# Kernel tuning notes

Measured on AMD Instinct MI355X. Metric: run time of the kernel, lower is better.

The kernel has to match this reference:

```python
import jax, jax.numpy as jnp
import numpy as np

N = 100000      # nodes
E = 1600000     # edges (avg degree 16)
F_IN = 128      # num_node_features
H = 64          # hidden_features
C = 40          # num_classes


def _glorot(key, shape):
    lim = np.sqrt(6.0 / (shape[0] + shape[1]))
    return jax.random.uniform(key, shape, jnp.float32, -lim, lim)


def setup_inputs() -> dict:
    key = jax.random.key(0)
    k = jax.random.split(key, 4)
    x = jax.random.normal(k[0], (N, F_IN), dtype=jnp.float32)
    edge_index = jax.random.randint(k[1], (2, E), 0, N, dtype=jnp.int32)
    W1 = _glorot(k[2], (F_IN, H))
    b1 = jnp.zeros((H,), jnp.float32)
    W2 = _glorot(k[3], (H, C))
    b2 = jnp.zeros((C,), jnp.float32)
    return {"x": x, "edge_index": edge_index, "W1": W1, "b1": b1, "W2": W2, "b2": b2}


def _gcn_conv(x, src, dst, dinv_sqrt, W, b):
    # GCNConv: out = D^{-1/2} (A + I) D^{-1/2} (x W) + b
    h = x @ W                                        # [N, out]
    norm = dinv_sqrt[src] * dinv_sqrt[dst]           # [E+N]
    msg = h[src] * norm[:, None]                     # gather + scale
    agg = jax.ops.segment_sum(msg, dst, num_segments=N)
    return agg + b


def reference(x, edge_index, W1, b1, W2, b2):
    loop = jnp.arange(N, dtype=edge_index.dtype)
    src = jnp.concatenate([edge_index[0], loop])     # add self-loops
    dst = jnp.concatenate([edge_index[1], loop])
    # degree of A + I (counts in-edges at destination, incl. self-loop)
    deg = jax.ops.segment_sum(jnp.ones_like(dst, jnp.float32), dst, num_segments=N)
    dinv_sqrt = jax.lax.rsqrt(deg)                   # deg >= 1 due to self-loops

    h = _gcn_conv(x, src, dst, dinv_sqrt, W1, b1)
    h = jax.nn.relu(h)
    # F.dropout(training=self.training) is identity in eval mode
    out = _gcn_conv(h, src, dst, dinv_sqrt, W2, b2)
    return out
```

## Files before the change

### kernel.cpp

```cpp
#include <hip/hip_runtime.h>
#include <hip/hip_fp16.h>
#include <cstdint>
#include <cstddef>

#define NPB_SHIFT 8
#define NPB (1 << NPB_SHIFT)
#define CHUNK 4096
#define BCAP 6144

typedef _Float16 half8_t __attribute__((ext_vector_type(8)));
typedef _Float16 half4_t __attribute__((ext_vector_type(4)));
typedef _Float16 half2_t __attribute__((ext_vector_type(2)));
typedef float floatx4 __attribute__((ext_vector_type(4)));

#define H2(u) __builtin_bit_cast(half2_t, (u))


__global__ __launch_bounds__(256) void k_partition(const int* __restrict__ src,
                                                   const int* __restrict__ dst,
                                                   int* __restrict__ bfill,
                                                   unsigned* __restrict__ tmp,
                                                   int E, int nbuck) {
  __shared__ int cnt[512];
  __shared__ int lbase[512];
  __shared__ int gdelta[512];
  __shared__ int cur[512];
  __shared__ int ps[256];
  __shared__ unsigned sval[CHUNK];
  __shared__ unsigned short sbid[CHUNK];
  int tid = threadIdx.x;
  int cbase = blockIdx.x * CHUNK;
  for (int i = tid; i < 512; i += 256) cnt[i] = 0;
  __syncthreads();
  int s[16], d[16];
  bool valid[16];
#pragma unroll
  for (int u = 0; u < 16; ++u) {
    int e = cbase + u * 256 + tid;
    valid[u] = e < E;
    s[u] = valid[u] ? src[e] : 0;
    d[u] = valid[u] ? dst[e] : 0;
    if (valid[u]) atomicAdd(&cnt[d[u] >> NPB_SHIFT], 1);
  }
  __syncthreads();
  int c0 = cnt[2 * tid], c1 = cnt[2 * tid + 1];
  int p = c0 + c1;
  ps[tid] = p;
  __syncthreads();
  for (int off = 1; off < 256; off <<= 1) {
    int t = (tid >= off) ? ps[tid - off] : 0;
    __syncthreads();
    ps[tid] += t;
    __syncthreads();
  }
  int ep = ps[tid] - p;
  lbase[2 * tid] = ep;
  lbase[2 * tid + 1] = ep + c0;
  __syncthreads();
  for (int i = tid; i < 512; i += 256) {
    cur[i] = lbase[i];
    if (cnt[i]) gdelta[i] = atomicAdd(&bfill[i], cnt[i]) - lbase[i];
  }
  __syncthreads();
#pragma unroll
  for (int u = 0; u < 16; ++u) {
    if (valid[u]) {
      int b = d[u] >> NPB_SHIFT;
      int r = atomicAdd(&cur[b], 1);
      sval[r] = ((unsigned)s[u] << NPB_SHIFT) | (unsigned)(d[u] & (NPB - 1));
      sbid[r] = (unsigned short)b;
    }
  }
  __syncthreads();
  int nv = min(CHUNK, E - cbase);
  for (int i = tid; i < nv; i += 256) {
    unsigned v = sval[i];
    int b = sbid[i];
    tmp[(size_t)b * BCAP + (gdelta[b] + i)] = v;
  }
}

__global__ __launch_bounds__(256) void k_csr_build(const unsigned* __restrict__ tmp,
                                                   const int* __restrict__ bfill,
                                                   float* __restrict__ dinv,
                                                   int* __restrict__ offset,
                                                   int* __restrict__ ssrc,
                                                   int N, int E, int nbuck) {
  __shared__ int cnt[NPB];
  __shared__ int scan[NPB];
  __shared__ int fillL[NPB];
  __shared__ int bs[512];
  __shared__ int ps[256];
  int b = blockIdx.x, tid = threadIdx.x;
  int nbase = b << NPB_SHIFT;
  int nloc = min(NPB, N - nbase);
  cnt[tid] = 0;
  bs[tid] = (tid < nbuck) ? bfill[tid] : 0;
  bs[tid + 256] = (tid + 256 < nbuck) ? bfill[tid + 256] : 0;
  __syncthreads();
  int c0 = bs[2 * tid], c1 = bs[2 * tid + 1];
  int pp = c0 + c1;
  ps[tid] = pp;
  __syncthreads();
  for (int off = 1; off < 256; off <<= 1) {
    int t = (tid >= off) ? ps[tid - off] : 0;
    __syncthreads();
    ps[tid] += t;
    __syncthreads();
  }
  int ep = ps[tid] - pp;
  bs[2 * tid] = ep;
  bs[2 * tid + 1] = ep + c0;
  __syncthreads();
  int ebeg = bs[b];
  int cntB = bfill[b];
  int sbeg = b * BCAP;
  int send = sbeg + cntB;
  for (int j = sbeg + tid; j < send; j += 256) atomicAdd(&cnt[tmp[j] & (NPB - 1)], 1);
  __syncthreads();
  int v = cnt[tid];
  scan[tid] = v;
  __syncthreads();
  for (int off = 1; off < NPB; off <<= 1) {
    int t = (tid >= off) ? scan[tid - off] : 0;
    __syncthreads();
    scan[tid] += t;
    __syncthreads();
  }
  int myoff = ebeg + scan[tid] - v;
  fillL[tid] = myoff;
  if (tid < nloc) {
    offset[nbase + tid] = myoff;
    dinv[nbase + tid] = rsqrtf((float)(v + 1));
  }
  if (b == nbuck - 1 && tid == NPB - 1) offset[N] = ebeg + scan[tid];
  __syncthreads();
  int j = sbeg + tid;
  for (; j + 3 * 256 < send; j += 4 * 256) {
    unsigned p[4];
#pragma unroll
    for (int u = 0; u < 4; ++u) p[u] = tmp[j + u * 256];
#pragma unroll
    for (int u = 0; u < 4; ++u) {
      int pos = atomicAdd(&fillL[p[u] & (NPB - 1)], 1);
      ssrc[pos] = (int)(p[u] >> NPB_SHIFT);
    }
  }
  for (; j < send; j += 256) {
    unsigned p = tmp[j];
    int pos = atomicAdd(&fillL[p & (NPB - 1)], 1);
    ssrc[pos] = (int)(p >> NPB_SHIFT);
  }
}

template <int K, int COLS, int MT, int KC, int OS, typename XT>
__global__ __launch_bounds__(256) void k_gemm_mfma(const XT* __restrict__ x,
                                                   const float* __restrict__ W,
                                                   const float* __restrict__ dinv,
                                                   _Float16* __restrict__ out, int n) {
  int lane = threadIdx.x & 63;
  int quad = lane >> 4;
  int l15 = lane & 15;
  int gwave = (blockIdx.x * blockDim.x + threadIdx.x) >> 6;
  int nwave = (gridDim.x * blockDim.x) >> 6;
  int ntiles = (n + 15) >> 4;

  half8_t afrag[MT][KC];
#pragma unroll
  for (int m = 0; m < MT; ++m) {
    int colw = m * 16 + l15;
    if (colw > COLS - 1) colw = COLS - 1;
#pragma unroll
    for (int c = 0; c < KC; ++c) {
#pragma unroll
      for (int j = 0; j < 8; ++j) {
        int kk = c * 32 + quad * 8 + j;
        afrag[m][c][j] = (_Float16)W[kk * COLS + colw];
      }
    }
  }

  for (int tile = gwave; tile < ntiles; tile += nwave) {
    int node0 = tile << 4;
    int nodeB = node0 + l15;
    int nodeC = nodeB < n ? nodeB : n - 1;
    const XT* xr = x + (size_t)nodeC * K;
    float dv = dinv[nodeC];
    half8_t bfrag[KC];
#pragma unroll
    for (int c = 0; c < KC; ++c) {
      if constexpr (sizeof(XT) == 4) {
        float4 lo = *(const float4*)(xr + c * 32 + quad * 8);
        float4 hi = *(const float4*)(xr + c * 32 + quad * 8 + 4);
        bfrag[c][0] = (_Float16)lo.x; bfrag[c][1] = (_Float16)lo.y;
        bfrag[c][2] = (_Float16)lo.z; bfrag[c][3] = (_Float16)lo.w;
        bfrag[c][4] = (_Float16)hi.x; bfrag[c][5] = (_Float16)hi.y;
        bfrag[c][6] = (_Float16)hi.z; bfrag[c][7] = (_Float16)hi.w;
      } else {
        bfrag[c] = *(const half8_t*)(xr + c * 32 + quad * 8);
      }
    }
    floatx4 acc[MT];
#pragma unroll
    for (int m = 0; m < MT; ++m) acc[m] = (floatx4){0.f, 0.f, 0.f, 0.f};
#pragma unroll
    for (int c = 0; c < KC; ++c)
#pragma unroll
      for (int m = 0; m < MT; ++m)
        acc[m] = __builtin_amdgcn_mfma_f32_16x16x32_f16(afrag[m][c], bfrag[c], acc[m], 0, 0, 0);

    if (nodeB < n) {
#pragma unroll
      for (int m = 0; m < MT; ++m) {
        int colBase = m * 16 + quad * 4;
        if (colBase < COLS) {
          half4_t hv = {(_Float16)(acc[m][0] * dv), (_Float16)(acc[m][1] * dv),
                        (_Float16)(acc[m][2] * dv), (_Float16)(acc[m][3] * dv)};
          *(half4_t*)(out + (size_t)nodeB * OS + colBase) = hv;
        }
      }
    }
  }
}


__device__ __forceinline__ void addacc(half2_t* acc, uint4 r) {
  acc[0] += H2(r.x); acc[1] += H2(r.y); acc[2] += H2(r.z); acc[3] += H2(r.w);
}

template <int F, int S8, bool RELU, bool OUT_HALF>
__global__ __launch_bounds__(256) void k_agg_v4(const uint4* __restrict__ g8,
                                                const int* __restrict__ offset,
                                                const int* __restrict__ ssrc,
                                                const float* __restrict__ dinv,
                                                const float* __restrict__ bias,
                                                void* __restrict__ outp, int n) {
  constexpr int F8 = F / 8;
  int lane = threadIdx.x & 63;
  int g = lane >> 3;
  int t = lane & 7;
  int wave = (blockIdx.x * blockDim.x + threadIdx.x) >> 6;
  int nb = wave * 4;
  if (nb >= n) return;
  bool tv = t < F8;

  uint4 sv[4];
#pragma unroll
  for (int w = 0; w < 4; ++w) {
    int node = nb + w;
    int nc = node < n ? node : n - 1;
    sv[w] = (tv && g == 0 && node < n) ? g8[(size_t)nc * S8 + t]
                                       : make_uint4(0, 0, 0, 0);
  }

  int jj[4], ee[4];
  float di[4];
#pragma unroll
  for (int w = 0; w < 4; ++w) {
    int node = nb + w;
    bool nv = node < n;
    int nc = nv ? node : n - 1;
    int b0 = offset[nc];
    int b1 = offset[nc + 1];
    jj[w] = b0;
    ee[w] = nv ? b1 : b0;
    di[w] = dinv[nc];
  }

  half2_t acc[4][4];
#pragma unroll
  for (int w = 0; w < 4; ++w) {
#pragma unroll
    for (int k = 0; k < 4; ++k) acc[w][k] = H2(0u);
    addacc(acc[w], sv[w]);
  }

  for (;;) {
    bool a0[4], a1[4];
    bool any = false;
#pragma unroll
    for (int w = 0; w < 4; ++w) {
      a0[w] = jj[w] + 8 <= ee[w];
      a1[w] = jj[w] + 16 <= ee[w];
      any = any || a0[w];
    }
    if (!any) break;
    int s0[4], s1[4];
#pragma unroll
    for (int w = 0; w < 4; ++w) {
      s0[w] = a0[w] ? ssrc[jj[w] + g] : 0;
      s1[w] = a1[w] ? ssrc[jj[w] + 8 + g] : 0;
    }
    uint4 r0[4], r1[4];
#pragma unroll
    for (int w = 0; w < 4; ++w) {
      r0[w] = (a0[w] && tv) ? g8[(size_t)s0[w] * S8 + t] : make_uint4(0, 0, 0, 0);
      r1[w] = (a1[w] && tv) ? g8[(size_t)s1[w] * S8 + t] : make_uint4(0, 0, 0, 0);
    }
#pragma unroll
    for (int w = 0; w < 4; ++w) {
      addacc(acc[w], r0[w]);
      addacc(acc[w], r1[w]);
      jj[w] += a1[w] ? 16 : (a0[w] ? 8 : 0);
    }
  }

  {
    int rem[4];
    uint4 rv[4];
#pragma unroll
    for (int w = 0; w < 4; ++w) {
      rem[w] = ee[w] - jj[w];
      int gi = (g < rem[w]) ? g : (rem[w] - 1);
      int sW = rem[w] > 0 ? ssrc[jj[w] + gi] : 0;
      rv[w] = (tv && g < rem[w]) ? g8[(size_t)sW * S8 + t] : make_uint4(0, 0, 0, 0);
    }
#pragma unroll
    for (int w = 0; w < 4; ++w) addacc(acc[w], rv[w]);
  }

#pragma unroll
  for (int w = 0; w < 4; ++w) {
#pragma unroll
    for (int k = 0; k < 4; ++k) {
      int u = __builtin_bit_cast(int, acc[w][k]);
      acc[w][k] += H2((unsigned)__shfl_xor(u, 8));
      u = __builtin_bit_cast(int, acc[w][k]);
      acc[w][k] += H2((unsigned)__shfl_xor(u, 16));
      u = __builtin_bit_cast(int, acc[w][k]);
      acc[w][k] += H2((unsigned)__shfl_xor(u, 32));
    }
    int node = nb + w;
    if (node < n && lane < F8) {
      float f[8];
#pragma unroll
      for (int k = 0; k < 4; ++k) {
        f[2 * k] = (float)acc[w][k][0];
        f[2 * k + 1] = (float)acc[w][k][1];
      }
      const float* bb = bias + lane * 8;
      float o[8];
#pragma unroll
      for (int j = 0; j < 8; ++j) {
        o[j] = fmaf(f[j], di[w], bb[j]);
        if (RELU) o[j] = fmaxf(o[j], 0.f);
      }
      if (OUT_HALF) {
        _Float16* op = (_Float16*)outp + (size_t)node * F + lane * 8;
        half2_t p0 = {(_Float16)o[0], (_Float16)o[1]};
        half2_t p1 = {(_Float16)o[2], (_Float16)o[3]};
        half2_t p2 = {(_Float16)o[4], (_Float16)o[5]};
        half2_t p3 = {(_Float16)o[6], (_Float16)o[7]};
        uint4 wv;
        wv.x = __builtin_bit_cast(unsigned, p0);
        wv.y = __builtin_bit_cast(unsigned, p1);
        wv.z = __builtin_bit_cast(unsigned, p2);
        wv.w = __builtin_bit_cast(unsigned, p3);
        *(uint4*)op = wv;
      } else {
        float* op = (float*)outp + (size_t)node * F + lane * 8;
        *(float4*)op = make_float4(o[0], o[1], o[2], o[3]);
        *(float4*)(op + 4) = make_float4(o[4], o[5], o[6], o[7]);
      }
    }
  }
}


extern "C" void kernel_launch(void* const* d_in, const int* in_sizes, int n_in,
                              void* d_out, int out_size, void* d_ws, size_t ws_size,
                              hipStream_t stream) {
  const float* x  = (const float*)d_in[0];
  const int*   ei = (const int*)d_in[1];
  const float* W1 = (const float*)d_in[2];
  const float* b1 = (const float*)d_in[3];
  const float* W2 = (const float*)d_in[4];
  const float* b2 = (const float*)d_in[5];
  float* out = (float*)d_out;

  const int F_IN = 128, HID = 64, C = 40;
  int N = in_sizes[0] / F_IN;
  int E = in_sizes[1] / 2;
  const int* src = ei;
  const int* dst = ei + E;
  int nbuck = (N + NPB - 1) >> NPB_SHIFT;

  char* w = (char*)d_ws;
  size_t o = 0;
  auto alloc = [&](size_t bytes) -> void* {
    void* p = w + o;
    o = (o + bytes + 255) & ~(size_t)255;
    return p;
  };
  float*    dinv   = (float*)alloc((size_t)N * 4);
  int*      offset = (int*)alloc((size_t)(N + 1) * 4);
  int*      bfill  = (int*)alloc(512 * 4);
  unsigned* tmp    = (unsigned*)alloc((size_t)nbuck * BCAP * 4);
  int*      ssrc   = (int*)alloc((size_t)E * 4);
  _Float16* g1     = (_Float16*)alloc((size_t)N * HID * 2);
  _Float16* h1     = (_Float16*)alloc((size_t)N * HID * 2);
  _Float16* g2     = (_Float16*)alloc((size_t)N * C * 2);

  dim3 b256(256);

  hipMemsetAsync(bfill, 0, 512 * 4, stream);
  k_partition<<<dim3((E + CHUNK - 1) / CHUNK), b256, 0, stream>>>(src, dst, bfill, tmp, E, nbuck);
  k_csr_build<<<dim3(nbuck), b256, 0, stream>>>(tmp, bfill, dinv, offset, ssrc, N, E, nbuck);

  k_gemm_mfma<128, 64, 4, 4, 64, float><<<dim3(1536), b256, 0, stream>>>(x, W1, dinv, g1, N);
  k_agg_v4<64, 8, true, true><<<dim3((N + 15) / 16), b256, 0, stream>>>(
      (const uint4*)g1, offset, ssrc, dinv, b1, h1, N);

  k_gemm_mfma<64, 40, 3, 2, 40, _Float16><<<dim3(1536), b256, 0, stream>>>(h1, W2, dinv, g2, N);
  k_agg_v4<40, 5, false, false><<<dim3((N + 15) / 16), b256, 0, stream>>>(
      (const uint4*)g2, offset, ssrc, dinv, b2, out, N);
}
```

Measured before the change: 250.4 us.

## Fuse layer-1 aggregation with bias, ReLU and second-layer GEMM

Replaces the layer-1 aggregation kernel and the second MFMA GEMM with one kernel. After gathering neighbours, each wave reduces partial sums across lanes with shuffles, applies bias, ReLU and the degree scaling, then multiplies by W2 held in LDS using fdot2. This drops the h1 intermediate buffer, its write and read-back, and one kernel launch. The cost is a scalar dot-product path in place of matrix cores, plus extra shuffles per node.

```diff
diff --git a/kernel.cpp b/kernel.cpp
--- a/kernel.cpp
+++ b/kernel.cpp
@@ -228,6 +228,153 @@
   acc[0] += H2(r.x); acc[1] += H2(r.y); acc[2] += H2(r.z); acc[3] += H2(r.w);
 }
 
+__global__ __launch_bounds__(256) void k_agg_fuse(const uint4* __restrict__ g8,
+                                                  const int* __restrict__ offset,
+                                                  const int* __restrict__ ssrc,
+                                                  const float* __restrict__ dinv,
+                                                  const float* __restrict__ b1,
+                                                  const float* __restrict__ W2,
+                                                  _Float16* __restrict__ g2out,
+                                                  int n) {
+  constexpr int S8 = 8;
+  __shared__ unsigned w2h[64 * 36];
+  int tid = threadIdx.x;
+  for (int i = tid; i < 64 * 32; i += 256) {
+    int c = i >> 5, k2 = i & 31;
+    half2_t hv = {(_Float16)0.f, (_Float16)0.f};
+    if (c < 40) hv = half2_t{(_Float16)W2[(2 * k2) * 40 + c],
+                             (_Float16)W2[(2 * k2 + 1) * 40 + c]};
+    w2h[c * 36 + k2] = __builtin_bit_cast(unsigned, hv);
+  }
+  __syncthreads();
+
+  int lane = tid & 63;
+  int g = lane >> 3;
+  int t = lane & 7;
+  int wave = (blockIdx.x * blockDim.x + tid) >> 6;
+  int nb = wave * 4;
+  if (nb >= n) return;
+
+  uint4 sv[4];
+#pragma unroll
+  for (int w = 0; w < 4; ++w) {
+    int node = nb + w;
+    int nc = node < n ? node : n - 1;
+    sv[w] = (g == 0 && node < n) ? g8[(size_t)nc * S8 + t] : make_uint4(0, 0, 0, 0);
+  }
+
+  int jj[4], ee[4];
+  float di[4];
+#pragma unroll
+  for (int w = 0; w < 4; ++w) {
+    int node = nb + w;
+    bool nv = node < n;
+    int nc = nv ? node : n - 1;
+    int b0 = offset[nc];
+    int b1e = offset[nc + 1];
+    jj[w] = b0;
+    ee[w] = nv ? b1e : b0;
+    di[w] = dinv[nc];
+  }
+
+  half2_t acc[4][4];
+#pragma unroll
+  for (int w = 0; w < 4; ++w) {
+#pragma unroll
+    for (int k = 0; k < 4; ++k) acc[w][k] = H2(0u);
+    addacc(acc[w], sv[w]);
+  }
+
+  for (;;) {
+    bool a0[4], a1[4];
+    bool any = false;
+#pragma unroll
+    for (int w = 0; w < 4; ++w) {
+      a0[w] = jj[w] + 8 <= ee[w];
+      a1[w] = jj[w] + 16 <= ee[w];
+      any = any || a0[w];
+    }
+    if (!any) break;
+    int s0[4], s1[4];
+#pragma unroll
+    for (int w = 0; w < 4; ++w) {
+      s0[w] = a0[w] ? ssrc[jj[w] + g] : 0;
+      s1[w] = a1[w] ? ssrc[jj[w] + 8 + g] : 0;
+    }
+    uint4 r0[4], r1[4];
+#pragma unroll
+    for (int w = 0; w < 4; ++w) {
+      r0[w] = a0[w] ? g8[(size_t)s0[w] * S8 + t] : make_uint4(0, 0, 0, 0);
+      r1[w] = a1[w] ? g8[(size_t)s1[w] * S8 + t] : make_uint4(0, 0, 0, 0);
+    }
+#pragma unroll
+    for (int w = 0; w < 4; ++w) {
+      addacc(acc[w], r0[w]);
+      addacc(acc[w], r1[w]);
+      jj[w] += a1[w] ? 16 : (a0[w] ? 8 : 0);
+    }
+  }
+
+  {
+    int rem[4];
+    uint4 rv[4];
+#pragma unroll
+    for (int w = 0; w < 4; ++w) {
+      rem[w] = ee[w] - jj[w];
+      int gi = (g < rem[w]) ? g : (rem[w] - 1);
+      int sW = rem[w] > 0 ? ssrc[jj[w] + gi] : 0;
+      rv[w] = (g < rem[w]) ? g8[(size_t)sW * S8 + t] : make_uint4(0, 0, 0, 0);
+    }
+#pragma unroll
+    for (int w = 0; w < 4; ++w) addacc(acc[w], rv[w]);
+  }
+
+  int c = lane;
+  const unsigned* w2r = &w2h[c * 36];
+#pragma unroll
+  for (int w = 0; w < 4; ++w) {
+#pragma unroll
+    for (int k = 0; k < 4; ++k) {
+      int u = __builtin_bit_cast(int, acc[w][k]);
+      acc[w][k] += H2((unsigned)__shfl_xor(u, 8));
+      u = __builtin_bit_cast(int, acc[w][k]);
+      acc[w][k] += H2((unsigned)__shfl_xor(u, 16));
+      u = __builtin_bit_cast(int, acc[w][k]);
+      acc[w][k] += H2((unsigned)__shfl_xor(u, 32));
+    }
+    int node = nb + w;
+    float f[8];
+#pragma unroll
+    for (int k = 0; k < 4; ++k) {
+      f[2 * k] = (float)acc[w][k][0];
+      f[2 * k + 1] = (float)acc[w][k][1];
+    }
+    const float* bb = b1 + t * 8;
+    int oh[4];
+#pragma unroll
+    for (int k = 0; k < 4; ++k) {
+      float e0 = fmaxf(fmaf(f[2 * k], di[w], bb[2 * k]), 0.f);
+      float e1 = fmaxf(fmaf(f[2 * k + 1], di[w], bb[2 * k + 1]), 0.f);
+      half2_t hp = {(_Float16)e0, (_Float16)e1};
+      oh[k] = __builtin_bit_cast(int, hp);
+    }
+    float a2 = 0.f;
+#pragma unroll
+    for (int kk = 0; kk < 8; ++kk) {
+      uint4 wv = *(const uint4*)(w2r + kk * 4);
+#pragma unroll
+      for (int i = 0; i < 4; ++i) {
+        int m = kk * 4 + i;
+        int hb = __shfl(oh[m & 3], m >> 2);
+        unsigned wu = (&wv.x)[i];
+        a2 = __builtin_amdgcn_fdot2(H2((unsigned)hb), H2(wu), a2, false);
+      }
+    }
+    if (node < n && c < 40)
+      g2out[(size_t)node * 40 + c] = (_Float16)(di[w] * a2);
+  }
+}
+
 template <int F, int S8, bool RELU, bool OUT_HALF>
 __global__ __launch_bounds__(256) void k_agg_v4(const uint4* __restrict__ g8,
                                                 const int* __restrict__ offset,
@@ -398,7 +545,6 @@
   unsigned* tmp    = (unsigned*)alloc((size_t)nbuck * BCAP * 4);
   int*      ssrc   = (int*)alloc((size_t)E * 4);
   _Float16* g1     = (_Float16*)alloc((size_t)N * HID * 2);
-  _Float16* h1     = (_Float16*)alloc((size_t)N * HID * 2);
   _Float16* g2     = (_Float16*)alloc((size_t)N * C * 2);
 
   dim3 b256(256);
@@ -408,10 +554,10 @@
   k_csr_build<<<dim3(nbuck), b256, 0, stream>>>(tmp, bfill, dinv, offset, ssrc, N, E, nbuck);
 
   k_gemm_mfma<128, 64, 4, 4, 64, float><<<dim3(1536), b256, 0, stream>>>(x, W1, dinv, g1, N);
-  k_agg_v4<64, 8, true, true><<<dim3((N + 15) / 16), b256, 0, stream>>>(
-      (const uint4*)g1, offset, ssrc, dinv, b1, h1, N);
-
-  k_gemm_mfma<64, 40, 3, 2, 40, _Float16><<<dim3(1536), b256, 0, stream>>>(h1, W2, dinv, g2, N);
+
+  k_agg_fuse<<<dim3((N + 15) / 16), b256, 0, stream>>>(
+      (const uint4*)g1, offset, ssrc, dinv, b1, W2, g2, N);
+
   k_agg_v4<40, 5, false, false><<<dim3((N + 15) / 16), b256, 0, stream>>>(
       (const uint4*)g2, offset, ssrc, dinv, b2, out, N);
 }
```

Result: slower. 294.7 us (+17.7%).

## Store layer-1 features in feature-slice-major layout and aggregate per slice

Applied to the files above, without the earlier changes.

The first GEMM now writes its fp16 output as eight 8-feature slices, each contiguous over nodes. A new aggregation kernel gives each block one slice and 32 nodes, so the random neighbor gathers within a block hit a 1.6 MB slice that fits better in cache. The second GEMM reads the transposed h1 layout directly. The trade-off is that each neighbor index list is now read eight times (once per slice), and the 16-byte gathers become more scattered across the slice-major layout.

```diff
diff --git a/kernel.cpp b/kernel.cpp
--- a/kernel.cpp
+++ b/kernel.cpp
@@ -153,7 +153,7 @@
   }
 }
 
-template <int K, int COLS, int MT, int KC, int OS, typename XT>
+template <int K, int COLS, int MT, int KC, int OS, bool TLOAD, bool TSTORE, typename XT>
 __global__ __launch_bounds__(256) void k_gemm_mfma(const XT* __restrict__ x,
                                                    const float* __restrict__ W,
                                                    const float* __restrict__ dinv,
@@ -184,12 +184,16 @@
     int node0 = tile << 4;
     int nodeB = node0 + l15;
     int nodeC = nodeB < n ? nodeB : n - 1;
-    const XT* xr = x + (size_t)nodeC * K;
     float dv = dinv[nodeC];
     half8_t bfrag[KC];
 #pragma unroll
     for (int c = 0; c < KC; ++c) {
-      if constexpr (sizeof(XT) == 4) {
+      if constexpr (TLOAD) {
+        const _Float16* hr = (const _Float16*)x +
+                             ((size_t)(4 * c + quad) * n + nodeC) * 8;
+        bfrag[c] = *(const half8_t*)hr;
+      } else if constexpr (sizeof(XT) == 4) {
+        const XT* xr = x + (size_t)nodeC * K;
         float4 lo = *(const float4*)(xr + c * 32 + quad * 8);
         float4 hi = *(const float4*)(xr + c * 32 + quad * 8 + 4);
         bfrag[c][0] = (_Float16)lo.x; bfrag[c][1] = (_Float16)lo.y;
@@ -197,6 +201,7 @@
         bfrag[c][4] = (_Float16)hi.x; bfrag[c][5] = (_Float16)hi.y;
         bfrag[c][6] = (_Float16)hi.z; bfrag[c][7] = (_Float16)hi.w;
       } else {
+        const XT* xr = x + (size_t)nodeC * K;
         bfrag[c] = *(const half8_t*)(xr + c * 32 + quad * 8);
       }
     }
@@ -216,16 +221,95 @@
         if (colBase < COLS) {
           half4_t hv = {(_Float16)(acc[m][0] * dv), (_Float16)(acc[m][1] * dv),
                         (_Float16)(acc[m][2] * dv), (_Float16)(acc[m][3] * dv)};
-          *(half4_t*)(out + (size_t)nodeB * OS + colBase) = hv;
+          if constexpr (TSTORE) {
+            int sl = colBase >> 3, c8 = colBase & 7;
+            *(half4_t*)(out + ((size_t)sl * n + nodeB) * 8 + c8) = hv;
+          } else {
+            *(half4_t*)(out + (size_t)nodeB * OS + colBase) = hv;
+          }
         }
       }
     }
   }
 }
 
-
 __device__ __forceinline__ void addacc(half2_t* acc, uint4 r) {
   acc[0] += H2(r.x); acc[1] += H2(r.y); acc[2] += H2(r.z); acc[3] += H2(r.w);
+}
+
+__global__ __launch_bounds__(256) void k_agg_slice(const uint4* __restrict__ g1t,
+                                                   const int* __restrict__ offset,
+                                                   const int* __restrict__ ssrc,
+                                                   const float* __restrict__ dinv,
+                                                   const float* __restrict__ b1,
+                                                   _Float16* __restrict__ h1t,
+                                                   int n) {
+  int bid = blockIdx.x;
+  int t = bid & 7;
+  int nblk = bid >> 3;
+  int tid = threadIdx.x;
+  int lane = tid & 63;
+  int g = lane >> 3;
+  int node = nblk * 32 + (tid >> 6) * 8 + (lane & 7);
+  bool nv = node < n;
+  int nc = nv ? node : n - 1;
+  const uint4* gt = g1t + (size_t)t * n;
+
+  int jj = offset[nc];
+  int ee = nv ? offset[nc + 1] : jj;
+
+  half2_t acc[4];
+#pragma unroll
+  for (int k = 0; k < 4; ++k) acc[k] = H2(0u);
+  if (g == 0 && nv) addacc(acc, gt[nc]);
+
+  int j = jj + g;
+  if (j < ee) {
+    int scur = ssrc[j];
+    for (;;) {
+      int jn = j + 8;
+      int snxt = (jn < ee) ? ssrc[jn] : 0;
+      uint4 r = gt[scur];
+      addacc(acc, r);
+      j = jn;
+      if (j >= ee) break;
+      scur = snxt;
+    }
+  }
+
+#pragma unroll
+  for (int k = 0; k < 4; ++k) {
+    int u = __builtin_bit_cast(int, acc[k]);
+    acc[k] += H2((unsigned)__shfl_xor(u, 8));
+    u = __builtin_bit_cast(int, acc[k]);
+    acc[k] += H2((unsigned)__shfl_xor(u, 16));
+    u = __builtin_bit_cast(int, acc[k]);
+    acc[k] += H2((unsigned)__shfl_xor(u, 32));
+  }
+
+  if (g == 0 && nv) {
+    float di = dinv[node];
+    float f[8];
+#pragma unroll
+    for (int k = 0; k < 4; ++k) {
+      f[2 * k] = (float)acc[k][0];
+      f[2 * k + 1] = (float)acc[k][1];
+    }
+    const float* bb = b1 + t * 8;
+    half2_t p[4];
+#pragma unroll
+    for (int k = 0; k < 4; ++k) {
+      float e0 = fmaxf(fmaf(f[2 * k], di, bb[2 * k]), 0.f);
+      float e1 = fmaxf(fmaf(f[2 * k + 1], di, bb[2 * k + 1]), 0.f);
+      p[k] = half2_t{(_Float16)e0, (_Float16)e1};
+    }
+    uint4 wv;
+    wv.x = __builtin_bit_cast(unsigned, p[0]);
+    wv.y = __builtin_bit_cast(unsigned, p[1]);
+    wv.z = __builtin_bit_cast(unsigned, p[2]);
+    wv.w = __builtin_bit_cast(unsigned, p[3]);
+    *(uint4*)(h1t + ((size_t)t * n + node) * 8) = wv;
+  }
 }
 
 template <int F, int S8, bool RELU, bool OUT_HALF>
@@ -397,8 +481,8 @@
   int*      bfill  = (int*)alloc(512 * 4);
   unsigned* tmp    = (unsigned*)alloc((size_t)nbuck * BCAP * 4);
   int*      ssrc   = (int*)alloc((size_t)E * 4);
-  _Float16* g1     = (_Float16*)alloc((size_t)N * HID * 2);
-  _Float16* h1     = (_Float16*)alloc((size_t)N * HID * 2);
+  _Float16* g1t    = (_Float16*)alloc((size_t)N * HID * 2);
+  _Float16* h1t    = (_Float16*)alloc((size_t)N * HID * 2);
   _Float16* g2     = (_Float16*)alloc((size_t)N * C * 2);
 
   dim3 b256(256);
@@ -407,11 +491,13 @@
   k_partition<<<dim3((E + CHUNK - 1) / CHUNK), b256, 0, stream>>>(src, dst, bfill, tmp, E, nbuck);
   k_csr_build<<<dim3(nbuck), b256, 0, stream>>>(tmp, bfill, dinv, offset, ssrc, N, E, nbuck);
 
-  k_gemm_mfma<128, 64, 4, 4, 64, float><<<dim3(1536), b256, 0, stream>>>(x, W1, dinv, g1, N);
-  k_agg_v4<64, 8, true, true><<<dim3((N + 15) / 16), b256, 0, stream>>>(
-      (const uint4*)g1, offset, ssrc, dinv, b1, h1, N);
-
-  k_gemm_mfma<64, 40, 3, 2, 40, _Float16><<<dim3(1536), b256, 0, stream>>>(h1, W2, dinv, g2, N);
+  k_gemm_mfma<128, 64, 4, 4, 64, false, true, float><<<dim3(1536), b256, 0, stream>>>(
+      x, W1, dinv, g1t, N);
+  k_agg_slice<<<dim3(((N + 31) / 32) * 8), b256, 0, stream>>>(
+      (const uint4*)g1t, offset, ssrc, dinv, b1, h1t, N);
+
+  k_gemm_mfma<64, 40, 3, 2, 40, true, false, _Float16><<<dim3(1536), b256, 0, stream>>>(
+      h1t, W2, dinv, g2, N);
   k_agg_v4<40, 5, false, false><<<dim3((N + 15) / 16), b256, 0, stream>>>(
       (const uint4*)g2, offset, ssrc, dinv, b2, out, N);
 }
```

Result: slower. 265.5 us (+6.0%).
